# Kernel optimization log

Measured on AMD Instinct MI355X. Metric: run time of the kernel, lower is better.

## Reference

```python
import jax, jax.numpy as jnp
import numpy as np

N_NODES = 50000
N_EDGES = 640000
RANK = 128
ORDER = 3
N_GRAPHS = 50
LN_EPS = 1e-5


def setup_inputs() -> dict:
    key = jax.random.key(0)
    ks = jax.random.split(key, 8)
    features = jax.random.normal(ks[0], (N_NODES, RANK), dtype=jnp.float32)
    src = jax.random.randint(ks[1], (N_EDGES,), 0, N_NODES, dtype=jnp.int32)
    dst = jax.random.randint(ks[2], (N_EDGES,), 0, N_NODES, dtype=jnp.int32)
    batch_num_nodes = jnp.full((N_GRAPHS,), N_NODES // N_GRAPHS, dtype=jnp.int32)
    scale = 1.0 / np.sqrt(RANK)
    Ws = jax.random.normal(ks[3], (ORDER, RANK, RANK), dtype=jnp.float32) * scale
    bs = jnp.zeros((ORDER, RANK), dtype=jnp.float32)
    gammas = jnp.ones((ORDER, RANK), dtype=jnp.float32)
    betas = jnp.zeros((ORDER, RANK), dtype=jnp.float32)
    return {"features": features, "src": src, "dst": dst,
            "batch_num_nodes": batch_num_nodes,
            "Ws": Ws, "bs": bs, "gammas": gammas, "betas": betas}


def _layer_norm(x, gamma, beta):
    mu = jnp.mean(x, axis=-1, keepdims=True)
    var = jnp.mean(jnp.square(x - mu), axis=-1, keepdims=True)
    return (x - mu) * jax.lax.rsqrt(var + LN_EPS) * gamma + beta


def reference(features, src, dst, batch_num_nodes, Ws, bs, gammas, betas):
    ones = jnp.ones((src.shape[0],), dtype=features.dtype)
    deg_out = jax.ops.segment_sum(ones, src, num_segments=N_NODES)  # out-degree of src nodes
    deg_in = jax.ops.segment_sum(ones, dst, num_segments=N_NODES)   # in-degree of dst nodes
    inv_sqrt_out = jax.lax.rsqrt(jnp.maximum(deg_out, 1.0))[:, None]
    inv_sqrt_in = jax.lax.rsqrt(jnp.maximum(deg_in, 1.0))[:, None]

    feats = features
    for i in range(ORDER):
        # DGL GraphConv, norm='both': h = D_in^{-1/2} A D_out^{-1/2} (X W) + b
        h = (feats @ Ws[i]) * inv_sqrt_out
        agg = jax.ops.segment_sum(h[src], dst, num_segments=N_NODES)
        h = agg * inv_sqrt_in + bs[i]
        h = _layer_norm(h, gammas[i], betas[i])
        feats = jax.nn.relu(h)  # dropout is identity at inference

    first_idx = jnp.cumsum(jnp.concatenate([jnp.zeros((1,), jnp.int32), batch_num_nodes[:-1]]))
    return feats[first_idx]
```

## Files before the change

kernel.cpp:

```cpp
#include <hip/hip_runtime.h>

#define RANK 128
#define LN_EPS 1e-5f

#define NCH 4
#define CHUNK 12800
#define BINS (NCH * CHUNK)
#define ECH 64
#define BT 1024

using short8 = __attribute__((ext_vector_type(8))) short;
using v4f    = __attribute__((ext_vector_type(4))) float;

__device__ inline unsigned short f2bf(float f) {
    unsigned u = __float_as_uint(f);
    unsigned r = (u + 0x7FFF + ((u >> 16) & 1)) >> 16;
    return (unsigned short)r;
}

__global__ __launch_bounds__(BT) void hist_part(const int* __restrict__ src,
                                                const int* __restrict__ dst,
                                                int* __restrict__ pdst,
                                                int* __restrict__ psrc, int nE) {
    __shared__ int h[CHUNK];
    int c = blockIdx.x, n = blockIdx.y, z = blockIdx.z;
    const int* arr = z ? src : dst;
    int* pout = z ? psrc : pdst;
    int base = n * CHUNK;
    for (int i = threadIdx.x; i < CHUNK; i += BT) h[i] = 0;
    __syncthreads();
    int epc = (nE + ECH - 1) / ECH;
    int e0 = c * epc, e1 = min(e0 + epc, nE);
    for (int e = e0 + (int)threadIdx.x; e < e1; e += BT) {
        int v = arr[e] - base;
        if ((unsigned)v < (unsigned)CHUNK) atomicAdd(&h[v], 1);
    }
    __syncthreads();
    int* o = pout + (size_t)c * BINS + base;
    for (int i = threadIdx.x; i < CHUNK; i += BT) o[i] = h[i];
}

__global__ void reduce_part(const int* __restrict__ pdst, const int* __restrict__ psrc,
                            int* __restrict__ counts, float* __restrict__ invin,
                            float* __restrict__ invout, int M) {
    int b = blockIdx.x * blockDim.x + threadIdx.x;
    if (b >= M) return;
    int cd = 0, cs = 0;
#pragma unroll 8
    for (int c = 0; c < ECH; c++) {
        cd += pdst[(size_t)c * BINS + b];
        cs += psrc[(size_t)c * BINS + b];
    }
    counts[b] = cd;
    invin[b]  = rsqrtf(fmaxf((float)cd, 1.0f));
    invout[b] = rsqrtf(fmaxf((float)cs, 1.0f));
}

__global__ __launch_bounds__(256) void scan1_kernel(const int* __restrict__ counts,
                                                    int* __restrict__ ends,
                                                    int* __restrict__ bsums, int n) {
    __shared__ int tmp[256];
    int tid = threadIdx.x;
    int gid = blockIdx.x * 256 + tid;
    int v = (gid < n) ? counts[gid] : 0;
    tmp[tid] = v;
    __syncthreads();
    for (int off = 1; off < 256; off <<= 1) {
        int t = (tid >= off) ? tmp[tid - off] : 0;
        __syncthreads();
        tmp[tid] += t;
        __syncthreads();
    }
    if (gid < n) ends[gid] = tmp[tid];
    if (tid == 255) bsums[blockIdx.x] = tmp[255];
}

__global__ __launch_bounds__(256) void scan2_kernel(int* __restrict__ bsums, int nb) {
    __shared__ int tmp[256];
    int tid = threadIdx.x;
    int v = (tid < nb) ? bsums[tid] : 0;
    tmp[tid] = v;
    __syncthreads();
    for (int off = 1; off < 256; off <<= 1) {
        int t = (tid >= off) ? tmp[tid - off] : 0;
        __syncthreads();
        tmp[tid] += t;
        __syncthreads();
    }
    if (tid < nb) bsums[tid] = tmp[tid] - v;
}

__global__ __launch_bounds__(256) void scan3_kernel(int* __restrict__ ends,
                                                    const int* __restrict__ bsums, int n) {
    int gid = blockIdx.x * 256 + threadIdx.x;
    if (gid < n) ends[gid] += bsums[blockIdx.x];
}

__global__ void offs_kernel(int* __restrict__ pdst, const int* __restrict__ ends,
                            const int* __restrict__ counts, int M) {
    int b = blockIdx.x * blockDim.x + threadIdx.x;
    if (b >= M) return;
    int run = ends[b] - counts[b];
#pragma unroll 8
    for (int c = 0; c < ECH; c++) {
        size_t idx = (size_t)c * BINS + b;
        int t = pdst[idx];
        pdst[idx] = run;
        run += t;
    }
}

__global__ __launch_bounds__(BT) void fill_sorted(const int* __restrict__ src,
                                                  const int* __restrict__ dst,
                                                  const int* __restrict__ pdst,
                                                  int* __restrict__ csr_src, int nE) {
    __shared__ int cur[CHUNK];
    int c = blockIdx.x, n = blockIdx.y;
    int base = n * CHUNK;
    const int* o = pdst + (size_t)c * BINS + base;
    for (int i = threadIdx.x; i < CHUNK; i += BT) cur[i] = o[i];
    __syncthreads();
    int epc = (nE + ECH - 1) / ECH;
    int e0 = c * epc, e1 = min(e0 + epc, nE);
    for (int e = e0 + (int)threadIdx.x; e < e1; e += BT) {
        int d = dst[e] - base;
        if ((unsigned)d < (unsigned)CHUNK) {
            int pos = atomicAdd(&cur[d], 1);
            csr_src[pos] = src[e];
        }
    }
}

__global__ void mark3_kernel(const int* __restrict__ bnn, int nG,
                             int* __restrict__ T3, unsigned* __restrict__ bm3,
                             int* __restrict__ cnt3) {
    int lane = threadIdx.x & 63;
    if (nG <= 64) {
        int v = (lane < nG) ? bnn[lane] : 0;
        int orig = v;
#pragma unroll
        for (int off = 1; off < 64; off <<= 1) {
            int t = __shfl_up(v, off);
            if (lane >= off) v += t;
        }
        int excl = v - orig;
        if (lane < nG) {
            T3[lane] = excl;
            atomicOr(&bm3[excl >> 5], 1u << (excl & 31));
        }
        if (lane == 0) *cnt3 = nG;
    } else if (lane == 0) {
        int idx = 0;
        for (int g = 0; g < nG; g++) {
            T3[g] = idx;
            atomicOr(&bm3[idx >> 5], 1u << (idx & 31));
            idx += bnn[g];
        }
        *cnt3 = nG;
    }
}

__global__ __launch_bounds__(256) void frontier_csr(const int* __restrict__ list,
                                                    const int* __restrict__ cnt,
                                                    const int* __restrict__ ends,
                                                    const int* __restrict__ csr_src,
                                                    unsigned* __restrict__ bm_out,
                                                    int* __restrict__ out_list,
                                                    int* __restrict__ out_cnt) {
    int lane = threadIdx.x & 63;
    int wg = blockIdx.x * 4 + (threadIdx.x >> 6);
    int nW = gridDim.x * 4;
    int n = *cnt;
    for (int i = wg; i < n; i += nW) {
        int node = list[i];
        int end = ends[node];
        int beg = (node == 0) ? 0 : ends[node - 1];
        for (int e0 = beg; e0 < end; e0 += 64) {
            int u = 0;
            bool flag = false;
            if (e0 + lane < end) {
                u = csr_src[e0 + lane];
                unsigned old = atomicOr(&bm_out[u >> 5], 1u << (u & 31));
                flag = !((old >> (u & 31)) & 1);
            }
            unsigned long long mask = __ballot(flag);
            if (mask) {
                int leader = __ffsll((long long)mask) - 1;
                int base = 0;
                if (lane == leader) base = atomicAdd(out_cnt, __popcll(mask));
                base = __shfl(base, leader);
                if (flag) out_list[base + __popcll(mask & ((1ull << lane) - 1))] = u;
            }
        }
    }
}

__global__ void convert_scale(const float* __restrict__ X, const float* __restrict__ invout,
                              unsigned* __restrict__ Xs, int n2) {
    int i = blockIdx.x * blockDim.x + threadIdx.x;
    if (i < n2) {
        float s = invout[i >> 6];
        float2 v = ((const float2*)X)[i];
        Xs[i] = (unsigned)f2bf(v.x * s) | ((unsigned)f2bf(v.y * s) << 16);
    }
}

__global__ void repack_kernel(const float* __restrict__ Ws, short* __restrict__ Wt) {
    int l = blockIdx.x >> 3;
    int s = (blockIdx.x & 7) * 256 + threadIdx.x;
    int lane = s & 63, ct = (s >> 6) & 7, k0 = s >> 9;
    int m = lane & 15, quad = lane >> 4;
    const float* W = Ws + (size_t)l * RANK * RANK;
    short* o = Wt + (size_t)l * 16384 + (size_t)s * 8;
#pragma unroll
    for (int j = 0; j < 8; j++)
        o[j] = (short)f2bf(W[(k0 * 32 + quad * 8 + j) * RANK + ct * 16 + m]);
}

__global__ __launch_bounds__(256) void gather_agg(const unsigned* __restrict__ Fin,
                                                  const int* __restrict__ ends,
                                                  const int* __restrict__ csr_src,
                                                  const int* __restrict__ list,
                                                  const int* __restrict__ cnt,
                                                  unsigned* __restrict__ AG) {
    int lane = threadIdx.x & 63;
    int wg = blockIdx.x * 4 + (threadIdx.x >> 6);
    int nW = gridDim.x * 4;
    int seg = lane >> 4, m = lane & 15;
    int n = *cnt;

    for (int i = wg; i < n; i += nW) {
        int node = list[i];
        int end = ends[node];
        int e = (node == 0) ? 0 : ends[node - 1];

        float ax[8];
#pragma unroll
        for (int k = 0; k < 8; k++) ax[k] = 0.f;

        while (e < end) {
            int rem = end - e;
            int myi = 0;
            if (lane < rem) myi = csr_src[e + lane];
            int nn = min(rem, 64);
            int t = 0;
            for (; t + 16 <= nn; t += 16) {
                uint4 u[4];
#pragma unroll
                for (int gi = 0; gi < 4; gi++) {
                    int idx = __shfl(myi, t + gi * 4 + seg);
                    u[gi] = *(const uint4*)(Fin + (size_t)idx * 64 + m * 4);
                }
#pragma unroll
                for (int gi = 0; gi < 4; gi++) {
                    ax[0] += __uint_as_float(u[gi].x << 16);
                    ax[1] += __uint_as_float(u[gi].x & 0xFFFF0000u);
                    ax[2] += __uint_as_float(u[gi].y << 16);
                    ax[3] += __uint_as_float(u[gi].y & 0xFFFF0000u);
                    ax[4] += __uint_as_float(u[gi].z << 16);
                    ax[5] += __uint_as_float(u[gi].z & 0xFFFF0000u);
                    ax[6] += __uint_as_float(u[gi].w << 16);
                    ax[7] += __uint_as_float(u[gi].w & 0xFFFF0000u);
                }
            }
            for (; t < nn; t += 4) {
                bool act = (t + seg) < nn;
                int idx = __shfl(myi, (t + seg) & 63);
                if (act) {
                    uint4 u = *(const uint4*)(Fin + (size_t)idx * 64 + m * 4);
                    ax[0] += __uint_as_float(u.x << 16);
                    ax[1] += __uint_as_float(u.x & 0xFFFF0000u);
                    ax[2] += __uint_as_float(u.y << 16);
                    ax[3] += __uint_as_float(u.y & 0xFFFF0000u);
                    ax[4] += __uint_as_float(u.z << 16);
                    ax[5] += __uint_as_float(u.z & 0xFFFF0000u);
                    ax[6] += __uint_as_float(u.w << 16);
                    ax[7] += __uint_as_float(u.w & 0xFFFF0000u);
                }
            }
            e += nn;
        }

#pragma unroll
        for (int k = 0; k < 8; k++) {
            ax[k] += __shfl_xor(ax[k], 16);
            ax[k] += __shfl_xor(ax[k], 32);
        }
        if (seg == 0) {
            uint4 o;
            o.x = (unsigned)f2bf(ax[0]) | ((unsigned)f2bf(ax[1]) << 16);
            o.y = (unsigned)f2bf(ax[2]) | ((unsigned)f2bf(ax[3]) << 16);
            o.z = (unsigned)f2bf(ax[4]) | ((unsigned)f2bf(ax[5]) << 16);
            o.w = (unsigned)f2bf(ax[6]) | ((unsigned)f2bf(ax[7]) << 16);
            *(uint4*)(AG + (size_t)node * 64 + m * 4) = o;
        }
    }
}

template <int LAST>
__global__ __launch_bounds__(256) void gemm_ln(const short* __restrict__ AG,
                                               const short* __restrict__ Wt,
                                               const float* __restrict__ invin,
                                               const float* __restrict__ invout,
                                               const float* __restrict__ bias,
                                               const float* __restrict__ gamma,
                                               const float* __restrict__ beta,
                                               const int* __restrict__ list,
                                               const int* __restrict__ cnt,
                                               unsigned short* __restrict__ Fout,
                                               float* __restrict__ out) {
    int lane = threadIdx.x & 63;
    int m = lane & 15, quad = lane >> 4;
    int wg = blockIdx.x * 4 + (threadIdx.x >> 6);
    int nW = gridDim.x * 4;
    int n = *cnt;
    int tiles = (n + 15) >> 4;

    float bb[8], gg[8], pp[8];
#pragma unroll
    for (int ct = 0; ct < 8; ct++) {
        bb[ct] = bias[ct * 16 + m];
        gg[ct] = gamma[ct * 16 + m];
        pp[ct] = beta[ct * 16 + m];
    }

    for (int t = wg; t < tiles; t += nW) {
        int base = t * 16;
        int ra = min(base + m, n - 1);
        const short* arow = AG + (size_t)list[ra] * RANK + quad * 8;

        v4f acc[8];
#pragma unroll
        for (int ct = 0; ct < 8; ct++) acc[ct] = (v4f){0.f, 0.f, 0.f, 0.f};

#pragma unroll
        for (int k0 = 0; k0 < 4; k0++) {
            short8 a = *(const short8*)(arow + k0 * 32);
#pragma unroll
            for (int ct = 0; ct < 8; ct++) {
                short8 b = *(const short8*)(Wt + (size_t)((k0 * 8 + ct) * 64 + lane) * 8);
                acc[ct] = __builtin_amdgcn_mfma_f32_16x16x32_bf16(a, b, acc[ct], 0, 0, 0);
            }
        }

#pragma unroll
        for (int r = 0; r < 4; r++) {
            int gr = base + quad * 4 + r;
            bool valid = gr < n;
            int node = list[valid ? gr : (n - 1)];
            float iv = invin[node];
            float x[8];
            float sum = 0.f, sq = 0.f;
#pragma unroll
            for (int ct = 0; ct < 8; ct++) {
                float c = acc[ct][r] * iv + bb[ct];
                x[ct] = c;
                sum += c;
                sq += c * c;
            }
#pragma unroll
            for (int off = 1; off < 16; off <<= 1) {
                sum += __shfl_xor(sum, off);
                sq  += __shfl_xor(sq, off);
            }
            float mu = sum * (1.0f / RANK);
            float var = sq * (1.0f / RANK) - mu * mu;
            float rs = rsqrtf(var + LN_EPS);
            if (valid) {
                if (LAST) {
#pragma unroll
                    for (int ct = 0; ct < 8; ct++) {
                        float y = fmaxf((x[ct] - mu) * rs * gg[ct] + pp[ct], 0.f);
                        out[(size_t)gr * RANK + ct * 16 + m] = y;
                    }
                } else {
                    float so = invout[node];
#pragma unroll
                    for (int ct = 0; ct < 8; ct++) {
                        float y = fmaxf((x[ct] - mu) * rs * gg[ct] + pp[ct], 0.f);
                        Fout[(size_t)node * RANK + ct * 16 + m] = f2bf(y * so);
                    }
                }
            }
        }
    }
}

extern "C" void kernel_launch(void* const* d_in, const int* in_sizes, int n_in,
                              void* d_out, int out_size, void* d_ws, size_t ws_size,
                              hipStream_t stream) {
    const float* features = (const float*)d_in[0];
    const int* src = (const int*)d_in[1];
    const int* dst = (const int*)d_in[2];
    const int* bnn = (const int*)d_in[3];
    const float* Ws = (const float*)d_in[4];
    const float* bs = (const float*)d_in[5];
    const float* gammas = (const float*)d_in[6];
    const float* betas = (const float*)d_in[7];
    float* out = (float*)d_out;

    int M  = in_sizes[0] / RANK;
    int nE = in_sizes[1];
    int nG = in_sizes[3];
    int bmw = (M + 31) / 32;

    char* ws = (char*)d_ws;
    size_t off = 0;
    auto alloc = [&](size_t bytes) {
        void* p = ws + off;
        off += (bytes + 255) & ~(size_t)255;
        return p;
    };
    int*   counts  = (int*)alloc((size_t)M * 4);
    int*   ends    = (int*)alloc((size_t)M * 4);
    int*   bsums   = (int*)alloc(256 * 4);
    float* invout  = (float*)alloc((size_t)M * 4);
    float* invin   = (float*)alloc((size_t)M * 4);
    int*   csr_src = (int*)alloc((size_t)nE * 4);
    short* Wt      = (short*)alloc((size_t)3 * 16384 * 2);
    short* Xs      = (short*)alloc((size_t)M * RANK * 2);
    short* AG      = (short*)alloc((size_t)M * RANK * 2);
    short* F       = (short*)alloc((size_t)M * RANK * 2);
    int*   pdst    = (int*)alloc((size_t)ECH * BINS * 4);
    int*   psrc    = (int*)alloc((size_t)ECH * BINS * 4);
    char*  zbase   = (char*)alloc((size_t)(3 * bmw + 8) * 4);
    unsigned* bm3  = (unsigned*)zbase;
    unsigned* bm2  = bm3 + bmw;
    unsigned* bm1  = bm2 + bmw;
    int*   cnt2    = (int*)(bm1 + bmw);
    int*   cnt1    = cnt2 + 1;
    int*   cnt3    = (int*)alloc(256);
    int*   T3      = (int*)alloc((size_t)((nG + 63) & ~63) * 4);
    int*   T2      = (int*)alloc((size_t)M * 4);
    int*   T1      = (int*)alloc((size_t)M * 4);

    int nb = (M + 255) / 256;

    hipMemsetAsync(zbase, 0, (size_t)(3 * bmw + 8) * 4, stream);

    hist_part<<<dim3(ECH, NCH, 2), BT, 0, stream>>>(src, dst, pdst, psrc, nE);
    reduce_part<<<nb, 256, 0, stream>>>(pdst, psrc, counts, invin, invout, M);
    scan1_kernel<<<nb, 256, 0, stream>>>(counts, ends, bsums, M);
    scan2_kernel<<<1, 256, 0, stream>>>(bsums, nb);
    scan3_kernel<<<nb, 256, 0, stream>>>(ends, bsums, M);
    offs_kernel<<<nb, 256, 0, stream>>>(pdst, ends, counts, M);
    fill_sorted<<<dim3(ECH, NCH), BT, 0, stream>>>(src, dst, pdst, csr_src, nE);

    mark3_kernel<<<1, 64, 0, stream>>>(bnn, nG, T3, bm3, cnt3);
    frontier_csr<<<16, 256, 0, stream>>>(T3, cnt3, ends, csr_src, bm2, T2, cnt2);
    frontier_csr<<<64, 256, 0, stream>>>(T2, cnt2, ends, csr_src, bm1, T1, cnt1);

    repack_kernel<<<24, 256, 0, stream>>>(Ws, Wt);
    convert_scale<<<(M * 64 + 255) / 256, 256, 0, stream>>>(features, invout, (unsigned*)Xs, M * 64);

    gather_agg<<<256, 256, 0, stream>>>((const unsigned*)Xs, ends, csr_src, T1, cnt1, (unsigned*)AG);
    gemm_ln<0><<<128, 256, 0, stream>>>(AG, Wt, invin, invout,
                                        bs, gammas, betas, T1, cnt1, (unsigned short*)F, nullptr);
    gather_agg<<<64, 256, 0, stream>>>((const unsigned*)F, ends, csr_src, T2, cnt2, (unsigned*)AG);
    gemm_ln<0><<<16, 256, 0, stream>>>(AG, Wt + 16384, invin, invout,
                                       bs + RANK, gammas + RANK, betas + RANK, T2, cnt2,
                                       (unsigned short*)F, nullptr);
    gather_agg<<<16, 256, 0, stream>>>((const unsigned*)F, ends, csr_src, T3, cnt3, (unsigned*)AG);
    gemm_ln<1><<<1, 256, 0, stream>>>(AG, Wt + 32768, invin, invout,
                                      bs + 2 * RANK, gammas + 2 * RANK, betas + 2 * RANK, T3, cnt3,
                                      nullptr, out);
}
```

Baseline: 201.7 us.

## Fuse gather-aggregate with GEMM+LayerNorm and merge scan/setup kernels

Merges the gather-aggregate and the GEMM+LayerNorm kernels into one per-layer kernel that stages 16 aggregated rows in shared memory and splits the output columns across four waves. This drops the AG round-trip through global memory. It also folds the scan and offset kernels into two launches, combines the weight repack with the feature conversion, and replaces the first frontier expansion with a single-block kernel that uses a shared-memory bitmap. The goal is fewer launches and less global traffic, at the cost of extra block-level syncs per tile and less parallelism in the single-block frontier step.

Result: faster. 191.4 us (-5.1%).

```diff
diff --git a/kernel.cpp b/kernel.cpp
--- a/kernel.cpp
+++ b/kernel.cpp
@@ -8,6 +8,7 @@
 #define BINS (NCH * CHUNK)
 #define ECH 64
 #define BT 1024
+#define BMWL ((BINS + 31) / 32)
 
 using short8 = __attribute__((ext_vector_type(8))) short;
 using v4f    = __attribute__((ext_vector_type(4))) float;
@@ -40,30 +41,28 @@
     for (int i = threadIdx.x; i < CHUNK; i += BT) o[i] = h[i];
 }
 
-__global__ void reduce_part(const int* __restrict__ pdst, const int* __restrict__ psrc,
-                            int* __restrict__ counts, float* __restrict__ invin,
-                            float* __restrict__ invout, int M) {
-    int b = blockIdx.x * blockDim.x + threadIdx.x;
-    if (b >= M) return;
-    int cd = 0, cs = 0;
-#pragma unroll 8
-    for (int c = 0; c < ECH; c++) {
-        cd += pdst[(size_t)c * BINS + b];
-        cs += psrc[(size_t)c * BINS + b];
-    }
-    counts[b] = cd;
-    invin[b]  = rsqrtf(fmaxf((float)cd, 1.0f));
-    invout[b] = rsqrtf(fmaxf((float)cs, 1.0f));
-}
-
-__global__ __launch_bounds__(256) void scan1_kernel(const int* __restrict__ counts,
+__global__ __launch_bounds__(256) void reduce_scan1(const int* __restrict__ pdst,
+                                                    const int* __restrict__ psrc,
+                                                    int* __restrict__ counts,
+                                                    float* __restrict__ invin,
+                                                    float* __restrict__ invout,
                                                     int* __restrict__ ends,
-                                                    int* __restrict__ bsums, int n) {
+                                                    int* __restrict__ bsums, int M) {
     __shared__ int tmp[256];
     int tid = threadIdx.x;
     int gid = blockIdx.x * 256 + tid;
-    int v = (gid < n) ? counts[gid] : 0;
-    tmp[tid] = v;
+    int cd = 0, cs = 0;
+    if (gid < M) {
+#pragma unroll 8
+        for (int c = 0; c < ECH; c++) {
+            cd += pdst[(size_t)c * BINS + gid];
+            cs += psrc[(size_t)c * BINS + gid];
+        }
+        counts[gid] = cd;
+        invin[gid]  = rsqrtf(fmaxf((float)cd, 1.0f));
+        invout[gid] = rsqrtf(fmaxf((float)cs, 1.0f));
+    }
+    tmp[tid] = cd;
     __syncthreads();
     for (int off = 1; off < 256; off <<= 1) {
         int t = (tid >= off) ? tmp[tid - off] : 0;
@@ -71,42 +70,36 @@
         tmp[tid] += t;
         __syncthreads();
     }
-    if (gid < n) ends[gid] = tmp[tid];
+    if (gid < M) ends[gid] = tmp[tid];
     if (tid == 255) bsums[blockIdx.x] = tmp[255];
 }
 
-__global__ __launch_bounds__(256) void scan2_kernel(int* __restrict__ bsums, int nb) {
-    __shared__ int tmp[256];
+__global__ __launch_bounds__(256) void scan23_offs(int* __restrict__ ends,
+                                                   const int* __restrict__ counts,
+                                                   const int* __restrict__ bsums,
+                                                   int* __restrict__ pdst, int nb, int M) {
+    __shared__ int red[256];
     int tid = threadIdx.x;
-    int v = (tid < nb) ? bsums[tid] : 0;
-    tmp[tid] = v;
-    __syncthreads();
-    for (int off = 1; off < 256; off <<= 1) {
-        int t = (tid >= off) ? tmp[tid - off] : 0;
-        __syncthreads();
-        tmp[tid] += t;
-        __syncthreads();
-    }
-    if (tid < nb) bsums[tid] = tmp[tid] - v;
-}
-
-__global__ __launch_bounds__(256) void scan3_kernel(int* __restrict__ ends,
-                                                    const int* __restrict__ bsums, int n) {
-    int gid = blockIdx.x * 256 + threadIdx.x;
-    if (gid < n) ends[gid] += bsums[blockIdx.x];
-}
-
-__global__ void offs_kernel(int* __restrict__ pdst, const int* __restrict__ ends,
-                            const int* __restrict__ counts, int M) {
-    int b = blockIdx.x * blockDim.x + threadIdx.x;
-    if (b >= M) return;
-    int run = ends[b] - counts[b];
+    int b = blockIdx.x;
+    red[tid] = (tid < b && tid < nb) ? bsums[tid] : 0;
+    __syncthreads();
+    for (int off = 128; off > 0; off >>= 1) {
+        if (tid < off) red[tid] += red[tid + off];
+        __syncthreads();
+    }
+    int prefix = red[0];
+    int gid = b * 256 + tid;
+    if (gid < M) {
+        int e = ends[gid] + prefix;
+        ends[gid] = e;
+        int run = e - counts[gid];
 #pragma unroll 8
-    for (int c = 0; c < ECH; c++) {
-        size_t idx = (size_t)c * BINS + b;
-        int t = pdst[idx];
-        pdst[idx] = run;
-        run += t;
+        for (int c = 0; c < ECH; c++) {
+            size_t idx = (size_t)c * BINS + gid;
+            int t = pdst[idx];
+            pdst[idx] = run;
+            run += t;
+        }
     }
 }
 
@@ -131,33 +124,55 @@
     }
 }
 
-__global__ void mark3_kernel(const int* __restrict__ bnn, int nG,
-                             int* __restrict__ T3, unsigned* __restrict__ bm3,
-                             int* __restrict__ cnt3) {
-    int lane = threadIdx.x & 63;
-    if (nG <= 64) {
-        int v = (lane < nG) ? bnn[lane] : 0;
-        int orig = v;
-#pragma unroll
-        for (int off = 1; off < 64; off <<= 1) {
-            int t = __shfl_up(v, off);
-            if (lane >= off) v += t;
-        }
-        int excl = v - orig;
-        if (lane < nG) {
-            T3[lane] = excl;
-            atomicOr(&bm3[excl >> 5], 1u << (excl & 31));
-        }
-        if (lane == 0) *cnt3 = nG;
-    } else if (lane == 0) {
-        int idx = 0;
-        for (int g = 0; g < nG; g++) {
-            T3[g] = idx;
-            atomicOr(&bm3[idx >> 5], 1u << (idx & 31));
-            idx += bnn[g];
-        }
-        *cnt3 = nG;
-    }
+__global__ __launch_bounds__(256) void mark_expand3(const int* __restrict__ bnn, int nG,
+                                                    const int* __restrict__ ends,
+                                                    const int* __restrict__ csr_src,
+                                                    int* __restrict__ T3, int* __restrict__ cnt3,
+                                                    int* __restrict__ T2, int* __restrict__ cnt2) {
+    __shared__ unsigned bm[BMWL];
+    __shared__ int lcnt;
+    int tid = threadIdx.x;
+    for (int i = tid; i < BMWL; i += 256) bm[i] = 0;
+    if (tid == 0) lcnt = 0;
+    __syncthreads();
+    if (tid < 64) {
+        int lane = tid;
+        if (nG <= 64) {
+            int v = (lane < nG) ? bnn[lane] : 0;
+            int orig = v;
+#pragma unroll
+            for (int off = 1; off < 64; off <<= 1) {
+                int t = __shfl_up(v, off);
+                if (lane >= off) v += t;
+            }
+            int excl = v - orig;
+            if (lane < nG) T3[lane] = excl;
+            if (lane == 0) *cnt3 = nG;
+        } else if (lane == 0) {
+            int idx = 0;
+            for (int g = 0; g < nG; g++) { T3[g] = idx; idx += bnn[g]; }
+            *cnt3 = nG;
+        }
+    }
+    __syncthreads();
+    int lane = tid & 63, w = tid >> 6;
+    for (int i = w; i < nG; i += 4) {
+        int node = T3[i];
+        int end = ends[node];
+        int beg = (node == 0) ? 0 : ends[node - 1];
+        for (int e0 = beg; e0 < end; e0 += 64) {
+            if (e0 + lane < end) {
+                int u = csr_src[e0 + lane];
+                unsigned old = atomicOr(&bm[u >> 5], 1u << (u & 31));
+                if (!((old >> (u & 31)) & 1)) {
+                    int pos = atomicAdd(&lcnt, 1);
+                    T2[pos] = u;
+                }
+            }
+        }
+    }
+    __syncthreads();
+    if (tid == 0) *cnt2 = lcnt;
 }
 
 __global__ __launch_bounds__(256) void frontier_csr(const int* __restrict__ list,
@@ -195,194 +210,201 @@
     }
 }
 
-__global__ void convert_scale(const float* __restrict__ X, const float* __restrict__ invout,
-                              unsigned* __restrict__ Xs, int n2) {
-    int i = blockIdx.x * blockDim.x + threadIdx.x;
-    if (i < n2) {
-        float s = invout[i >> 6];
-        float2 v = ((const float2*)X)[i];
-        Xs[i] = (unsigned)f2bf(v.x * s) | ((unsigned)f2bf(v.y * s) << 16);
-    }
-}
-
-__global__ void repack_kernel(const float* __restrict__ Ws, short* __restrict__ Wt) {
-    int l = blockIdx.x >> 3;
-    int s = (blockIdx.x & 7) * 256 + threadIdx.x;
-    int lane = s & 63, ct = (s >> 6) & 7, k0 = s >> 9;
-    int m = lane & 15, quad = lane >> 4;
-    const float* W = Ws + (size_t)l * RANK * RANK;
-    short* o = Wt + (size_t)l * 16384 + (size_t)s * 8;
-#pragma unroll
-    for (int j = 0; j < 8; j++)
-        o[j] = (short)f2bf(W[(k0 * 32 + quad * 8 + j) * RANK + ct * 16 + m]);
-}
-
-__global__ __launch_bounds__(256) void gather_agg(const unsigned* __restrict__ Fin,
-                                                  const int* __restrict__ ends,
-                                                  const int* __restrict__ csr_src,
-                                                  const int* __restrict__ list,
-                                                  const int* __restrict__ cnt,
-                                                  unsigned* __restrict__ AG) {
-    int lane = threadIdx.x & 63;
-    int wg = blockIdx.x * 4 + (threadIdx.x >> 6);
-    int nW = gridDim.x * 4;
+__global__ __launch_bounds__(256) void repack_convert(const float* __restrict__ Ws,
+                                                      short* __restrict__ Wt,
+                                                      const float* __restrict__ X,
+                                                      const float* __restrict__ invout,
+                                                      unsigned* __restrict__ Xs, int n2) {
+    int bid = blockIdx.x;
+    if (bid < 24) {
+        int l = bid >> 3;
+        int s = (bid & 7) * 256 + threadIdx.x;
+        int lane = s & 63, ct = (s >> 6) & 7, k0 = s >> 9;
+        int m = lane & 15, quad = lane >> 4;
+        const float* W = Ws + (size_t)l * RANK * RANK;
+        short* o = Wt + (size_t)l * 16384 + (size_t)s * 8;
+#pragma unroll
+        for (int j = 0; j < 8; j++)
+            o[j] = (short)f2bf(W[(k0 * 32 + quad * 8 + j) * RANK + ct * 16 + m]);
+    } else {
+        int i = (bid - 24) * 256 + threadIdx.x;
+        if (i < n2) {
+            float s = invout[i >> 6];
+            float2 v = ((const float2*)X)[i];
+            Xs[i] = (unsigned)f2bf(v.x * s) | ((unsigned)f2bf(v.y * s) << 16);
+        }
+    }
+}
+
+template <int LAST>
+__global__ __launch_bounds__(256) void layer_fused(const unsigned* __restrict__ Fin,
+                                                   const int* __restrict__ ends,
+                                                   const int* __restrict__ csr_src,
+                                                   const short* __restrict__ Wt,
+                                                   const float* __restrict__ invin,
+                                                   const float* __restrict__ invout,
+                                                   const float* __restrict__ bias,
+                                                   const float* __restrict__ gamma,
+                                                   const float* __restrict__ beta,
+                                                   const int* __restrict__ list,
+                                                   const int* __restrict__ cnt,
+                                                   unsigned short* __restrict__ Fout,
+                                                   float* __restrict__ out) {
+    __shared__ short As[16][136];
+    __shared__ float sstat[2][4][16];
+    __shared__ float sinv[2][16];
+    __shared__ int snode[16];
+    int tid = threadIdx.x;
+    int w = tid >> 6, lane = tid & 63;
     int seg = lane >> 4, m = lane & 15;
     int n = *cnt;
-
-    for (int i = wg; i < n; i += nW) {
-        int node = list[i];
-        int end = ends[node];
-        int e = (node == 0) ? 0 : ends[node - 1];
-
-        float ax[8];
-#pragma unroll
-        for (int k = 0; k < 8; k++) ax[k] = 0.f;
-
-        while (e < end) {
-            int rem = end - e;
-            int myi = 0;
-            if (lane < rem) myi = csr_src[e + lane];
-            int nn = min(rem, 64);
-            int t = 0;
-            for (; t + 16 <= nn; t += 16) {
-                uint4 u[4];
-#pragma unroll
-                for (int gi = 0; gi < 4; gi++) {
-                    int idx = __shfl(myi, t + gi * 4 + seg);
-                    u[gi] = *(const uint4*)(Fin + (size_t)idx * 64 + m * 4);
+    int tiles = (n + 15) >> 4;
+
+    float bb[2], gg[2], pp[2];
+#pragma unroll
+    for (int j = 0; j < 2; j++) {
+        int col = (w * 2 + j) * 16 + m;
+        bb[j] = bias[col]; gg[j] = gamma[col]; pp[j] = beta[col];
+    }
+
+    for (int t = blockIdx.x; t < tiles; t += gridDim.x) {
+        int base = t * 16;
+
+        for (int q = 0; q < 4; q++) {
+            int rr = w * 4 + q;
+            int gr = base + rr;
+            float ax[8];
+#pragma unroll
+            for (int k = 0; k < 8; k++) ax[k] = 0.f;
+            int node = -1;
+            if (gr < n) {
+                node = list[gr];
+                int end = ends[node];
+                int e = (node == 0) ? 0 : ends[node - 1];
+                while (e < end) {
+                    int rem = end - e;
+                    int myi = 0;
+                    if (lane < rem) myi = csr_src[e + lane];
+                    int nn = min(rem, 64);
+                    int p = 0;
+                    for (; p + 16 <= nn; p += 16) {
+                        uint4 u[4];
+#pragma unroll
+                        for (int gi = 0; gi < 4; gi++) {
+                            int idx = __shfl(myi, p + gi * 4 + seg);
+                            u[gi] = *(const uint4*)(Fin + (size_t)idx * 64 + m * 4);
+                        }
+#pragma unroll
+                        for (int gi = 0; gi < 4; gi++) {
+                            ax[0] += __uint_as_float(u[gi].x << 16);
+                            ax[1] += __uint_as_float(u[gi].x & 0xFFFF0000u);
+                            ax[2] += __uint_as_float(u[gi].y << 16);
+                            ax[3] += __uint_as_float(u[gi].y & 0xFFFF0000u);
+                            ax[4] += __uint_as_float(u[gi].z << 16);
+                            ax[5] += __uint_as_float(u[gi].z & 0xFFFF0000u);
+                            ax[6] += __uint_as_float(u[gi].w << 16);
+                            ax[7] += __uint_as_float(u[gi].w & 0xFFFF0000u);
+                        }
+                    }
+                    for (; p < nn; p += 4) {
+                        bool act = (p + seg) < nn;
+                        int idx = __shfl(myi, (p + seg) & 63);
+                        if (act) {
+                            uint4 u = *(const uint4*)(Fin + (size_t)idx * 64 + m * 4);
+                            ax[0] += __uint_as_float(u.x << 16);
+                            ax[1] += __uint_as_float(u.x & 0xFFFF0000u);
+                            ax[2] += __uint_as_float(u.y << 16);
+                            ax[3] += __uint_as_float(u.y & 0xFFFF0000u);
+                            ax[4] += __uint_as_float(u.z << 16);
+                            ax[5] += __uint_as_float(u.z & 0xFFFF0000u);
+                            ax[6] += __uint_as_float(u.w << 16);
+                            ax[7] += __uint_as_float(u.w & 0xFFFF0000u);
+                        }
+                    }
+                    e += nn;
                 }
 #pragma unroll
-                for (int gi = 0; gi < 4; gi++) {
-                    ax[0] += __uint_as_float(u[gi].x << 16);
-                    ax[1] += __uint_as_float(u[gi].x & 0xFFFF0000u);
-                    ax[2] += __uint_as_float(u[gi].y << 16);
-                    ax[3] += __uint_as_float(u[gi].y & 0xFFFF0000u);
-                    ax[4] += __uint_as_float(u[gi].z << 16);
-                    ax[5] += __uint_as_float(u[gi].z & 0xFFFF0000u);
-                    ax[6] += __uint_as_float(u[gi].w << 16);
-                    ax[7] += __uint_as_float(u[gi].w & 0xFFFF0000u);
+                for (int k = 0; k < 8; k++) {
+                    ax[k] += __shfl_xor(ax[k], 16);
+                    ax[k] += __shfl_xor(ax[k], 32);
                 }
             }
-            for (; t < nn; t += 4) {
-                bool act = (t + seg) < nn;
-                int idx = __shfl(myi, (t + seg) & 63);
-                if (act) {
-                    uint4 u = *(const uint4*)(Fin + (size_t)idx * 64 + m * 4);
-                    ax[0] += __uint_as_float(u.x << 16);
-                    ax[1] += __uint_as_float(u.x & 0xFFFF0000u);
-                    ax[2] += __uint_as_float(u.y << 16);
-                    ax[3] += __uint_as_float(u.y & 0xFFFF0000u);
-                    ax[4] += __uint_as_float(u.z << 16);
-                    ax[5] += __uint_as_float(u.z & 0xFFFF0000u);
-                    ax[6] += __uint_as_float(u.w << 16);
-                    ax[7] += __uint_as_float(u.w & 0xFFFF0000u);
-                }
-            }
-            e += nn;
-        }
-
-#pragma unroll
-        for (int k = 0; k < 8; k++) {
-            ax[k] += __shfl_xor(ax[k], 16);
-            ax[k] += __shfl_xor(ax[k], 32);
-        }
-        if (seg == 0) {
-            uint4 o;
-            o.x = (unsigned)f2bf(ax[0]) | ((unsigned)f2bf(ax[1]) << 16);
-            o.y = (unsigned)f2bf(ax[2]) | ((unsigned)f2bf(ax[3]) << 16);
-            o.z = (unsigned)f2bf(ax[4]) | ((unsigned)f2bf(ax[5]) << 16);
-            o.w = (unsigned)f2bf(ax[6]) | ((unsigned)f2bf(ax[7]) << 16);
-            *(uint4*)(AG + (size_t)node * 64 + m * 4) = o;
-        }
-    }
-}
-
-template <int LAST>
-__global__ __launch_bounds__(256) void gemm_ln(const short* __restrict__ AG,
-                                               const short* __restrict__ Wt,
-                                               const float* __restrict__ invin,
-                                               const float* __restrict__ invout,
-                                               const float* __restrict__ bias,
-                                               const float* __restrict__ gamma,
-                                               const float* __restrict__ beta,
-                                               const int* __restrict__ list,
-                                               const int* __restrict__ cnt,
-                                               unsigned short* __restrict__ Fout,
-                                               float* __restrict__ out) {
-    int lane = threadIdx.x & 63;
-    int m = lane & 15, quad = lane >> 4;
-    int wg = blockIdx.x * 4 + (threadIdx.x >> 6);
-    int nW = gridDim.x * 4;
-    int n = *cnt;
-    int tiles = (n + 15) >> 4;
-
-    float bb[8], gg[8], pp[8];
-#pragma unroll
-    for (int ct = 0; ct < 8; ct++) {
-        bb[ct] = bias[ct * 16 + m];
-        gg[ct] = gamma[ct * 16 + m];
-        pp[ct] = beta[ct * 16 + m];
-    }
-
-    for (int t = wg; t < tiles; t += nW) {
-        int base = t * 16;
-        int ra = min(base + m, n - 1);
-        const short* arow = AG + (size_t)list[ra] * RANK + quad * 8;
-
-        v4f acc[8];
-#pragma unroll
-        for (int ct = 0; ct < 8; ct++) acc[ct] = (v4f){0.f, 0.f, 0.f, 0.f};
-
+            if (seg == 0) {
+                uint4 o;
+                o.x = (unsigned)f2bf(ax[0]) | ((unsigned)f2bf(ax[1]) << 16);
+                o.y = (unsigned)f2bf(ax[2]) | ((unsigned)f2bf(ax[3]) << 16);
+                o.z = (unsigned)f2bf(ax[4]) | ((unsigned)f2bf(ax[5]) << 16);
+                o.w = (unsigned)f2bf(ax[6]) | ((unsigned)f2bf(ax[7]) << 16);
+                *(uint4*)&As[rr][8 * m] = o;
+            }
+            if (lane == 0) {
+                snode[rr] = node;
+                sinv[0][rr] = (node >= 0) ? invin[node] : 1.f;
+                sinv[1][rr] = (node >= 0) ? invout[node] : 1.f;
+            }
+        }
+        __syncthreads();
+
+        short8 a[4];
+#pragma unroll
+        for (int k0 = 0; k0 < 4; k0++)
+            a[k0] = *(const short8*)&As[m][k0 * 32 + seg * 8];
+        v4f acc[2];
+        acc[0] = (v4f){0.f, 0.f, 0.f, 0.f};
+        acc[1] = (v4f){0.f, 0.f, 0.f, 0.f};
 #pragma unroll
         for (int k0 = 0; k0 < 4; k0++) {
-            short8 a = *(const short8*)(arow + k0 * 32);
-#pragma unroll
-            for (int ct = 0; ct < 8; ct++) {
+#pragma unroll
+            for (int j = 0; j < 2; j++) {
+                int ct = w * 2 + j;
                 short8 b = *(const short8*)(Wt + (size_t)((k0 * 8 + ct) * 64 + lane) * 8);
-                acc[ct] = __builtin_amdgcn_mfma_f32_16x16x32_bf16(a, b, acc[ct], 0, 0, 0);
-            }
-        }
-
+                acc[j] = __builtin_amdgcn_mfma_f32_16x16x32_bf16(a[k0], b, acc[j], 0, 0, 0);
+            }
+        }
+
+        float x[4][2];
 #pragma unroll
         for (int r = 0; r < 4; r++) {
-            int gr = base + quad * 4 + r;
-            bool valid = gr < n;
-            int node = list[valid ? gr : (n - 1)];
-            float iv = invin[node];
-            float x[8];
-            float sum = 0.f, sq = 0.f;
-#pragma unroll
-            for (int ct = 0; ct < 8; ct++) {
-                float c = acc[ct][r] * iv + bb[ct];
-                x[ct] = c;
-                sum += c;
-                sq += c * c;
+            int row = seg * 4 + r;
+            float iv = sinv[0][row];
+            float s = 0.f, sq = 0.f;
+#pragma unroll
+            for (int j = 0; j < 2; j++) {
+                float c = acc[j][r] * iv + bb[j];
+                x[r][j] = c;
+                s += c; sq += c * c;
             }
 #pragma unroll
             for (int off = 1; off < 16; off <<= 1) {
-                sum += __shfl_xor(sum, off);
-                sq  += __shfl_xor(sq, off);
-            }
-            float mu = sum * (1.0f / RANK);
+                s  += __shfl_xor(s, off);
+                sq += __shfl_xor(sq, off);
+            }
+            if (m == 0) { sstat[0][w][row] = s; sstat[1][w][row] = sq; }
+        }
+        __syncthreads();
+
+#pragma unroll
+        for (int r = 0; r < 4; r++) {
+            int row = seg * 4 + r;
+            int gr = base + row;
+            if (gr >= n) continue;
+            float s  = sstat[0][0][row] + sstat[0][1][row] + sstat[0][2][row] + sstat[0][3][row];
+            float sq = sstat[1][0][row] + sstat[1][1][row] + sstat[1][2][row] + sstat[1][3][row];
+            float mu = s * (1.0f / RANK);
             float var = sq * (1.0f / RANK) - mu * mu;
             float rs = rsqrtf(var + LN_EPS);
-            if (valid) {
+#pragma unroll
+            for (int j = 0; j < 2; j++) {
+                int col = (w * 2 + j) * 16 + m;
+                float y = fmaxf((x[r][j] - mu) * rs * gg[j] + pp[j], 0.f);
                 if (LAST) {
-#pragma unroll
-                    for (int ct = 0; ct < 8; ct++) {
-                        float y = fmaxf((x[ct] - mu) * rs * gg[ct] + pp[ct], 0.f);
-                        out[(size_t)gr * RANK + ct * 16 + m] = y;
-                    }
+                    out[(size_t)gr * RANK + col] = y;
                 } else {
-                    float so = invout[node];
-#pragma unroll
-                    for (int ct = 0; ct < 8; ct++) {
-                        float y = fmaxf((x[ct] - mu) * rs * gg[ct] + pp[ct], 0.f);
-                        Fout[(size_t)node * RANK + ct * 16 + m] = f2bf(y * so);
-                    }
+                    Fout[(size_t)snode[row] * RANK + col] = f2bf(y * sinv[1][row]);
                 }
             }
         }
+        __syncthreads();
     }
 }
 
@@ -419,16 +441,14 @@
     int*   csr_src = (int*)alloc((size_t)nE * 4);
     short* Wt      = (short*)alloc((size_t)3 * 16384 * 2);
     short* Xs      = (short*)alloc((size_t)M * RANK * 2);
-    short* AG      = (short*)alloc((size_t)M * RANK * 2);
-    short* F       = (short*)alloc((size_t)M * RANK * 2);
+    short* F1      = (short*)alloc((size_t)M * RANK * 2);
+    short* F2      = (short*)alloc((size_t)M * RANK * 2);
     int*   pdst    = (int*)alloc((size_t)ECH * BINS * 4);
     int*   psrc    = (int*)alloc((size_t)ECH * BINS * 4);
-    char*  zbase   = (char*)alloc((size_t)(3 * bmw + 8) * 4);
-    unsigned* bm3  = (unsigned*)zbase;
-    unsigned* bm2  = bm3 + bmw;
-    unsigned* bm1  = bm2 + bmw;
-    int*   cnt2    = (int*)(bm1 + bmw);
-    int*   cnt1    = cnt2 + 1;
+    char*  zbase   = (char*)alloc((size_t)(bmw + 1) * 4);
+    unsigned* bm1  = (unsigned*)zbase;
+    int*   cnt1    = (int*)(bm1 + bmw);
+    int*   cnt2    = (int*)alloc(256);
     int*   cnt3    = (int*)alloc(256);
     int*   T3      = (int*)alloc((size_t)((nG + 63) & ~63) * 4);
     int*   T2      = (int*)alloc((size_t)M * 4);
@@ -436,32 +456,27 @@
 
     int nb = (M + 255) / 256;
 
-    hipMemsetAsync(zbase, 0, (size_t)(3 * bmw + 8) * 4, stream);
+    hipMemsetAsync(zbase, 0, (size_t)(bmw + 1) * 4, stream);
 
     hist_part<<<dim3(ECH, NCH, 2), BT, 0, stream>>>(src, dst, pdst, psrc, nE);
-    reduce_part<<<nb, 256, 0, stream>>>(pdst, psrc, counts, invin, invout, M);
-    scan1_kernel<<<nb, 256, 0, stream>>>(counts, ends, bsums, M);
-    scan2_kernel<<<1, 256, 0, stream>>>(bsums, nb);
-    scan3_kernel<<<nb, 256, 0, stream>>>(ends, bsums, M);
-    offs_kernel<<<nb, 256, 0, stream>>>(pdst, ends, counts, M);
+    reduce_scan1<<<nb, 256, 0, stream>>>(pdst, psrc, counts, invin, invout, ends, bsums, M);
+    scan23_offs<<<nb, 256, 0, stream>>>(ends, counts, bsums, pdst, nb, M);
     fill_sorted<<<dim3(ECH, NCH), BT, 0, stream>>>(src, dst, pdst, csr_src, nE);
 
-    mark3_kernel<<<1, 64, 0, stream>>>(bnn, nG, T3, bm3, cnt3);
-    frontier_csr<<<16, 256, 0, stream>>>(T3, cnt3, ends, csr_src, bm2, T2, cnt2);
+    mark_expand3<<<1, 256, 0, stream>>>(bnn, nG, ends, csr_src, T3, cnt3, T2, cnt2);
     frontier_csr<<<64, 256, 0, stream>>>(T2, cnt2, ends, csr_src, bm1, T1, cnt1);
 
-    repack_kernel<<<24, 256, 0, stream>>>(Ws, Wt);
-    convert_scale<<<(M * 64 + 255) / 256, 256, 0, stream>>>(features, invout, (unsigned*)Xs, M * 64);
-
-    gather_agg<<<256, 256, 0, stream>>>((const unsigned*)Xs, ends, csr_src, T1, cnt1, (unsigned*)AG);
-    gemm_ln<0><<<128, 256, 0, stream>>>(AG, Wt, invin, invout,
-                                        bs, gammas, betas, T1, cnt1, (unsigned short*)F, nullptr);
-    gather_agg<<<64, 256, 0, stream>>>((const unsigned*)F, ends, csr_src, T2, cnt2, (unsigned*)AG);
-    gemm_ln<0><<<16, 256, 0, stream>>>(AG, Wt + 16384, invin, invout,
-                                       bs + RANK, gammas + RANK, betas + RANK, T2, cnt2,
-                                       (unsigned short*)F, nullptr);
-    gather_agg<<<16, 256, 0, stream>>>((const unsigned*)F, ends, csr_src, T3, cnt3, (unsigned*)AG);
-    gemm_ln<1><<<1, 256, 0, stream>>>(AG, Wt + 32768, invin, invout,
-                                      bs + 2 * RANK, gammas + 2 * RANK, betas + 2 * RANK, T3, cnt3,
-                                      nullptr, out);
-}
+    int cb = (M * 64 + 255) / 256;
+    repack_convert<<<24 + cb, 256, 0, stream>>>(Ws, Wt, features, invout, (unsigned*)Xs, M * 64);
+
+    layer_fused<0><<<512, 256, 0, stream>>>((const unsigned*)Xs, ends, csr_src, Wt,
+                                            invin, invout, bs, gammas, betas,
+                                            T1, cnt1, (unsigned short*)F1, nullptr);
+    layer_fused<0><<<64, 256, 0, stream>>>((const unsigned*)F1, ends, csr_src, Wt + 16384,
+                                           invin, invout, bs + RANK, gammas + RANK, betas + RANK,
+                                           T2, cnt2, (unsigned short*)F2, nullptr);
+    layer_fused<1><<<(nG + 15) / 16, 256, 0, stream>>>((const unsigned*)F2, ends, csr_src, Wt + 32768,
+                                                       invin, invout, bs + 2 * RANK,
+                                                       gammas + 2 * RANK, betas + 2 * RANK,
+                                                       T3, cnt3, nullptr, out);
+}
```
